# Optimization experiments

Measured on AMD Instinct MI355X. Metric: run time of the kernel, lower is better.

## Reference

```python
import math
import jax, jax.numpy as jnp
import numpy as np

B, T, C, H = 1, 2048, 1024, 16
D = C // H
ROPE_THETA = 10000.0


def rope_sin_cos(t, d, theta, dtype=jnp.float32):
    # (T, D/2) sin/cos tables, standard RoPE frequencies
    inv_freq = 1.0 / (theta ** (jnp.arange(0, d, 2, dtype=jnp.float32) / d))
    ang = jnp.arange(t, dtype=jnp.float32)[:, None] * inv_freq[None, :]  # (T, D/2)
    return jnp.sin(ang).astype(dtype), jnp.cos(ang).astype(dtype)


def apply_rope(x, sin, cos):
    # x: (B, H, T, D); rotate interleaved even/odd pairs
    x1 = x[..., 0::2]
    x2 = x[..., 1::2]
    s = sin[None, None, :, :]
    c = cos[None, None, :, :]
    r1 = x1 * c - x2 * s
    r2 = x1 * s + x2 * c
    # interleave back to (..., D)
    return jnp.stack([r1, r2], axis=-1).reshape(x.shape)


def setup_inputs() -> dict:
    key = jax.random.key(0)
    k1, k2, k3 = jax.random.split(key, 3)
    x = jax.random.normal(k1, (B, T, C), dtype=jnp.float32)
    w_qkv = jax.random.normal(k2, (C, 3 * C), dtype=jnp.float32) * (1.0 / math.sqrt(C))
    w_proj = jax.random.normal(k3, (C, C), dtype=jnp.float32) * (1.0 / math.sqrt(C))
    return {"x": x, "w_qkv": w_qkv, "w_proj": w_proj}


def reference(x, w_qkv, w_proj):
    b, t, c = x.shape
    qkv = x @ w_qkv                               # (B, T, 3C)
    qkv = qkv.reshape(b, t, 3, H, D)
    q = qkv[:, :, 0].transpose(0, 2, 1, 3)        # (B, H, T, D)
    k = qkv[:, :, 1].transpose(0, 2, 1, 3)
    v = qkv[:, :, 2].transpose(0, 2, 1, 3)

    sin, cos = rope_sin_cos(t, D, ROPE_THETA, dtype=x.dtype)
    q = apply_rope(q, sin, cos)
    k = apply_rope(k, sin, cos)

    scores = jnp.einsum('bhqd,bhkd->bhqk', q, k) * (1.0 / math.sqrt(D))
    causal = jnp.tril(jnp.ones((t, t), dtype=bool))
    scores = jnp.where(causal[None, None, :, :], scores, jnp.finfo(scores.dtype).min)
    probs = jax.nn.softmax(scores, axis=-1)       # (B, H, T, T)
    out = jnp.einsum('bhqk,bhkd->bhqd', probs, v)
    out = out.transpose(0, 2, 1, 3).reshape(b, t, c)
    return out @ w_proj
```

## Files before the change

### kernel.cpp

```cpp
#include <hip/hip_runtime.h>
#include <math.h>

#define TT 2048
#define CC 1024
#define HH 16
#define DD 64
#define N3 3072

typedef unsigned short u16;
typedef __bf16 bf16x8 __attribute__((ext_vector_type(8)));
typedef float f32x4 __attribute__((ext_vector_type(4)));
typedef unsigned short u16x8 __attribute__((ext_vector_type(8)));
typedef const __attribute__((address_space(1))) void gv_t;
typedef __attribute__((address_space(3))) void lv_t;

__device__ __forceinline__ u16 bf16_rne(float f) {
  unsigned u = __float_as_uint(f);
  u += 0x7FFFu + ((u >> 16) & 1u);
  return (u16)(u >> 16);
}
__device__ __forceinline__ float bf16f(u16 h) {
  return __uint_as_float(((unsigned)h) << 16);
}
__device__ __forceinline__ bf16x8 ldfrag(const u16* p) {
  return __builtin_bit_cast(bf16x8, *(const u16x8*)p);
}
#if __has_builtin(__builtin_amdgcn_cvt_pk_bf16_f32)
__device__ __forceinline__ unsigned pk_bf16(float a, float b) {
  return __builtin_bit_cast(unsigned, __builtin_amdgcn_cvt_pk_bf16_f32(a, b));
}
#else
__device__ __forceinline__ unsigned pk_bf16(float a, float b) {
  return (unsigned)bf16_rne(a) | ((unsigned)bf16_rne(b) << 16);
}
#endif

__global__ __launch_bounds__(256) void k_prep(
    const float* __restrict__ x, const float* __restrict__ w_qkv,
    const float* __restrict__ w_proj, u16* __restrict__ xb,
    u16* __restrict__ wqkvT, u16* __restrict__ wprojT,
    float2* __restrict__ scos ) {
  __shared__ u16 tile[64][34];
  const int bi = blockIdx.x, tid = threadIdx.x;
  if (bi < 2048) {
    int i = bi * 256 + tid;
    float4 v = ((const float4*)x)[i];
    ushort4 r;
    r.x = bf16_rne(v.x); r.y = bf16_rne(v.y); r.z = bf16_rne(v.z); r.w = bf16_rne(v.w);
    ((ushort4*)xb)[i] = r;
    return;
  }
  if (bi >= 2048 + 1536 + 512) {
    int idx = (bi - 4096) * 256 + tid;
    int t = idx >> 5, i = idx & 31;
    float inv_freq = exp2f(-(float)(2 * i) * (1.0f / 64.0f) * 13.2877123795494f);
    float ang = (float)t * inv_freq;
    scos[idx] = make_float2(sinf(ang), cosf(ang));
    return;
  }
  const float* w; u16* wt; int K, N, n0, k0;
  if (bi < 2048 + 1536) {
    int b = bi - 2048; w = w_qkv; wt = wqkvT; K = CC; N = N3;
    k0 = (b / 96) * 64; n0 = (b % 96) * 32;
  } else {
    int b = bi - 3584; w = w_proj; wt = wprojT; K = CC; N = CC;
    k0 = (b >> 5) * 64; n0 = (b & 31) * 32;
  }
  const int tx = tid & 31, r0 = tid >> 5;
#pragma unroll
  for (int j = 0; j < 8; j++) {
    int k = r0 + j * 8;
    tile[k][tx] = bf16_rne(w[(size_t)(k0 + k) * N + n0 + tx]);
  }
  __syncthreads();
  const int kc = tid & 15, nr = tid >> 4;
#pragma unroll
  for (int jn = 0; jn < 2; jn++) {
    int n = nr + (jn << 4);
    ushort4 o;
    o.x = tile[kc * 4 + 0][n];
    o.y = tile[kc * 4 + 1][n];
    o.z = tile[kc * 4 + 2][n];
    o.w = tile[kc * 4 + 3][n];
    *(ushort4*)&wt[(size_t)(n0 + n) * K + k0 + kc * 4] = o;
  }
}

__device__ __forceinline__ bf16x8 rdsw(const u16* base, int rr, int c8) {
  return ldfrag(&base[rr * 64 + ((c8 ^ (rr & 7)) << 3)]);
}

__global__ __launch_bounds__(256) void k_gemm_qkv(
    const u16* __restrict__ A, const u16* __restrict__ Bt,
    const float2* __restrict__ scos , u16* __restrict__ qr,
    u16* __restrict__ kr, u16* __restrict__ vt, int M, int N, int K) {
  __shared__ u16 As[2][128 * 64];
  __shared__ u16 Bs[2][96 * 64];
  const int tid = threadIdx.x;
  const int lane = tid & 63, w = tid >> 6;
  const int col = lane & 15, quad = lane >> 4;
  const int wm = w >> 1, wn = w & 1;
  const int tm = blockIdx.y * 128, tn = blockIdx.x * 96;

  const int lr = lane >> 3;
  const int soff = ((lane & 7) ^ lr) << 3;

  f32x4 acc[12];
#pragma unroll
  for (int i = 0; i < 12; i++) acc[i] = (f32x4){0.f, 0.f, 0.f, 0.f};

  auto stage = [&](int k0, int buf) {
#pragma unroll
    for (int i = 0; i < 4; i++) {
      const int rbase = w * 32 + i * 8;
      __builtin_amdgcn_global_load_lds(
          (gv_t*)(A + (size_t)(tm + rbase + lr) * K + k0 + soff),
          (lv_t*)(&As[buf][rbase * 64]), 16, 0, 0);
    }
#pragma unroll
    for (int i = 0; i < 3; i++) {
      const int rbase = w * 24 + i * 8;
      __builtin_amdgcn_global_load_lds(
          (gv_t*)(Bt + (size_t)(tn + rbase + lr) * K + k0 + soff),
          (lv_t*)(&Bs[buf][rbase * 64]), 16, 0, 0);
    }
  };

  stage(0, 0);
  __syncthreads();
  const int NT = K / 64;
  for (int t = 0; t < NT; t++) {
    const int cur = t & 1;
    if (t + 1 < NT) stage((t + 1) * 64, cur ^ 1);
#pragma unroll
    for (int kk = 0; kk < 2; kk++) {
      bf16x8 af[4], bf[3];
#pragma unroll
      for (int mt = 0; mt < 4; mt++)
        af[mt] = rdsw(&As[cur][0], wm * 64 + mt * 16 + col, kk * 4 + quad);
#pragma unroll
      for (int nt = 0; nt < 3; nt++)
        bf[nt] = rdsw(&Bs[cur][0], wn * 48 + nt * 16 + col, kk * 4 + quad);
#pragma unroll
      for (int mt = 0; mt < 4; mt++)
#pragma unroll
        for (int nt = 0; nt < 3; nt++)
          acc[mt * 3 + nt] = __builtin_amdgcn_mfma_f32_16x16x32_bf16(af[mt], bf[nt], acc[mt * 3 + nt], 0, 0, 0);
    }
    __syncthreads();
  }
  u16* scr = ((u16*)As) + w * 1088;

  const int tb = tm + wm * 64;
#pragma unroll
  for (int nt = 0; nt < 3; nt++) {
    const int nn = tn + wn * 48 + nt * 16;
    const int slice = nn >> 10;
    const int hh = (nn >> 6) & 15;
    const int db = nn & 63;
    const int d = db + col;
    if (slice < 2) {
      u16* dst = (slice == 0) ? qr : kr;
      const bool ev = (col & 1) == 0;
      const int i = (db >> 1) + (col >> 1);
#pragma unroll
      for (int mt = 0; mt < 4; mt++)
#pragma unroll
        for (int r = 0; r < 4; r++) {
          int t = tb + mt * 16 + quad * 4 + r;
          float2 sc2 = scos[t * 32 + i];
          float e = acc[mt * 3 + nt][r];
          float pp = __shfl_xor(e, 1);
          float v = ev ? (e * sc2.y - pp * sc2.x) : (pp * sc2.x + e * sc2.y);
          dst[((size_t)(hh * TT + t) << 6) + d] = bf16_rne(v);
        }
    } else {
#pragma unroll
      for (int mt = 0; mt < 4; mt++)
#pragma unroll
        for (int r = 0; r < 4; r++)
          scr[col * 68 + mt * 16 + quad * 4 + r] = bf16_rne(acc[mt * 3 + nt][r]);
#pragma unroll
      for (int i = 0; i < 4; i++) {
        const int dl = quad + i * 4;
        const int tl = col * 4;
        ushort4 vv = *(const ushort4*)&scr[dl * 68 + tl];
        *(ushort4*)&vt[((size_t)(hh * DD + db + dl)) * TT + tb + tl] = vv;
      }
    }
  }
}

__global__ __launch_bounds__(256) void k_gemm_pj(
    const u16* __restrict__ A, const u16* __restrict__ Bt,
    float* __restrict__ C, int M, int N, int K) {
  __shared__ u16 As[2][128 * 64];
  __shared__ u16 Bs[2][64 * 64];
  const int tid = threadIdx.x;
  const int lane = tid & 63, w = tid >> 6;
  const int col = lane & 15, quad = lane >> 4;
  const int tm = blockIdx.y * 128, tn = blockIdx.x * 64;

  const int lr = lane >> 3;
  const int soff = ((lane & 7) ^ lr) << 3;

  f32x4 acc[8];
#pragma unroll
  for (int i = 0; i < 8; i++) acc[i] = (f32x4){0.f, 0.f, 0.f, 0.f};

  auto stage = [&](int k0, int buf) {
#pragma unroll
    for (int i = 0; i < 4; i++) {
      const int rbase = w * 32 + i * 8;
      __builtin_amdgcn_global_load_lds(
          (gv_t*)(A + (size_t)(tm + rbase + lr) * K + k0 + soff),
          (lv_t*)(&As[buf][rbase * 64]), 16, 0, 0);
    }
#pragma unroll
    for (int i = 0; i < 2; i++) {
      const int rbase = w * 16 + i * 8;
      __builtin_amdgcn_global_load_lds(
          (gv_t*)(Bt + (size_t)(tn + rbase + lr) * K + k0 + soff),
          (lv_t*)(&Bs[buf][rbase * 64]), 16, 0, 0);
    }
  };

  stage(0, 0);
  __syncthreads();
  const int NT = K / 64;
  for (int t = 0; t < NT; t++) {
    const int cur = t & 1;
    if (t + 1 < NT) stage((t + 1) * 64, cur ^ 1);
#pragma unroll
    for (int kk = 0; kk < 2; kk++) {
      bf16x8 af[2], bf[4];
#pragma unroll
      for (int mt = 0; mt < 2; mt++)
        af[mt] = rdsw(&As[cur][0], w * 32 + mt * 16 + col, kk * 4 + quad);
#pragma unroll
      for (int nt = 0; nt < 4; nt++)
        bf[nt] = rdsw(&Bs[cur][0], nt * 16 + col, kk * 4 + quad);
#pragma unroll
      for (int mt = 0; mt < 2; mt++)
#pragma unroll
        for (int nt = 0; nt < 4; nt++)
          acc[mt * 4 + nt] = __builtin_amdgcn_mfma_f32_16x16x32_bf16(af[mt], bf[nt], acc[mt * 4 + nt], 0, 0, 0);
    }
    __syncthreads();
  }
#pragma unroll
  for (int mt = 0; mt < 2; mt++)
#pragma unroll
    for (int nt = 0; nt < 4; nt++)
#pragma unroll
      for (int r = 0; r < 4; r++)
        C[(size_t)(tm + w * 32 + mt * 16 + quad * 4 + r) * N + tn + nt * 16 + col] =
            acc[mt * 4 + nt][r];
}

__global__ __launch_bounds__(256) void k_flash(
    const u16* __restrict__ qr, const u16* __restrict__ kr,
    const u16* __restrict__ vt, u16* __restrict__ attnb ) {
  __shared__ u16 Ks[2][2][64 * 64];
  __shared__ u16 Vs[2][2][64 * 64];
  __shared__ u16 Ps[4][16 * 64];

  const int tid = threadIdx.x;
  const int lane = tid & 63, wv = tid >> 6;
  const int col = lane & 15, quad = lane >> 4;

  const int bid = blockIdx.x;
  const int xcd = bid & 7, slot = bid >> 3;
  const int cu = slot & 31, half = slot >> 5;
  const int rank = half ? (63 - cu) : cu;
  const int sp = 31 - (rank >> 1);
  const int h = xcd * 2 + (rank & 1);
  const int q0 = sp * 64;
  const int nkt = sp + 1;
  const int nw = (nkt + 1) >> 1;

  const u16* Qh = qr + (size_t)h * TT * DD;
  const u16* Kh = kr + (size_t)h * TT * DD;
  const u16* Vh = vt + (size_t)h * DD * TT;

  const bf16x8 aq0 = ldfrag(&Qh[(size_t)(q0 + wv * 16 + col) * DD + quad * 8]);
  const bf16x8 aq1 = ldfrag(&Qh[(size_t)(q0 + wv * 16 + col) * DD + 32 + quad * 8]);

  const int lr = lane >> 3;
  const int srcoff = ((lane & 7) ^ lr) << 3;

  auto stage = [&](int win, int buf) {
    const int k0 = win * 128;
#pragma unroll
    for (int j = 0; j < 2; j++) {
#pragma unroll
      for (int i = 0; i < 2; i++) {
        const int rbase = wv * 16 + i * 8;
        __builtin_amdgcn_global_load_lds(
            (gv_t*)(Kh + (size_t)(k0 + j * 64 + rbase + lr) * DD + srcoff),
            (lv_t*)(&Ks[buf][j][rbase * 64]), 16, 0, 0);
        __builtin_amdgcn_global_load_lds(
            (gv_t*)(Vh + (size_t)(rbase + lr) * TT + k0 + j * 64 + srcoff),
            (lv_t*)(&Vs[buf][j][rbase * 64]), 16, 0, 0);
      }
    }
  };

  const f32x4 zero = {0.f, 0.f, 0.f, 0.f};
  f32x4 acc[4] = {zero, zero, zero, zero};
  float lpart[4] = {0.f, 0.f, 0.f, 0.f};
  u16* Pb = &Ps[wv][0];

  auto compute = [&](int k0j, const u16* Kt, const u16* Vt) {
    f32x4 sc[4];
#pragma unroll
    for (int nt = 0; nt < 4; nt++) {
      const int rr = nt * 16 + col;
      sc[nt] = __builtin_amdgcn_mfma_f32_16x16x32_bf16(aq0, rdsw(Kt, rr, quad), zero, 0, 0, 0);
      sc[nt] = __builtin_amdgcn_mfma_f32_16x16x32_bf16(aq1, rdsw(Kt, rr, 4 + quad), sc[nt], 0, 0, 0);
    }
    if (k0j == q0) {
#pragma unroll
      for (int nt = 0; nt < 4; nt++)
#pragma unroll
        for (int r = 0; r < 4; r++)
          if (nt * 16 + col > wv * 16 + quad * 4 + r) sc[nt][r] = -1e30f;
    }
#pragma unroll
    for (int nt = 0; nt < 4; nt++)
#pragma unroll
      for (int r = 0; r < 4; r++) {
        float p = exp2f(fmaf(sc[nt][r], 0.18033688f, -28.8539008f));
        sc[nt][r] = p;
        lpart[r] += p;
      }
#pragma unroll
    for (int nt = 0; nt < 4; nt++) {
      unsigned p01 = pk_bf16(sc[nt][0], sc[nt][1]);
      unsigned p23 = pk_bf16(sc[nt][2], sc[nt][3]);
      u16* base = Pb + quad * 4 * 64 + ((nt ^ quad) << 4) + col;
      base[0 * 64] = (u16)p01;
      base[1 * 64] = (u16)(p01 >> 16);
      base[2 * 64] = (u16)p23;
      base[3 * 64] = (u16)(p23 >> 16);
    }
#pragma unroll
    for (int kk = 0; kk < 2; kk++) {
      int sb = (kk * 2 + (quad >> 1)) ^ (col >> 2);
      bf16x8 ap = ldfrag(&Pb[col * 64 + (sb << 4) + ((quad & 1) << 3)]);
#pragma unroll
      for (int nt = 0; nt < 4; nt++)
        acc[nt] = __builtin_amdgcn_mfma_f32_16x16x32_bf16(
            ap, rdsw(Vt, nt * 16 + col, kk * 4 + quad), acc[nt], 0, 0, 0);
    }
  };

  stage(0, 0);
  for (int win = 0; win < nw; win++) {
    const int buf = win & 1;
    __syncthreads();
    if (win + 1 < nw) stage(win + 1, buf ^ 1);
#pragma unroll
    for (int j = 0; j < 2; j++) {
      const int k0j = win * 128 + j * 64;
      if (k0j <= q0) compute(k0j, Ks[buf][j], Vs[buf][j]);
    }
  }

#pragma unroll
  for (int o = 1; o < 16; o <<= 1)
#pragma unroll
    for (int r = 0; r < 4; r++) lpart[r] += __shfl_xor(lpart[r], o);
  float inv[4];
#pragma unroll
  for (int r = 0; r < 4; r++) inv[r] = 1.f / lpart[r];
#pragma unroll
  for (int nt = 0; nt < 4; nt++)
#pragma unroll
    for (int r = 0; r < 4; r++) {
      int q = q0 + wv * 16 + quad * 4 + r;
      attnb[(size_t)q * CC + h * DD + nt * 16 + col] = bf16_rne(acc[nt][r] * inv[r]);
    }
}

extern "C" void kernel_launch(void* const* d_in, const int* in_sizes, int n_in,
                              void* d_out, int out_size, void* d_ws, size_t ws_size,
                              hipStream_t stream) {
  const float* x      = (const float*)d_in[0];
  const float* w_qkv  = (const float*)d_in[1];
  const float* w_proj = (const float*)d_in[2];
  float* out = (float*)d_out;

  char* p = (char*)d_ws;
  u16* xb      = (u16*)p;    p += (size_t)TT * CC * 2;
  u16* wqkvT   = (u16*)p;    p += (size_t)N3 * CC * 2;
  u16* wprojT  = (u16*)p;    p += (size_t)CC * CC * 2;
  float2* scos = (float2*)p; p += (size_t)TT * 32 * 8;
  u16* qr      = (u16*)p;    p += (size_t)HH * TT * DD * 2;
  u16* kr      = (u16*)p;    p += (size_t)HH * TT * DD * 2;
  u16* vt      = (u16*)p;    p += (size_t)HH * DD * TT * 2;
  u16* attnb   = (u16*)p;    p += (size_t)TT * CC * 2;

  k_prep<<<2048 + 1536 + 512 + 256, 256, 0, stream>>>(x, w_qkv, w_proj, xb, wqkvT, wprojT, scos);
  k_gemm_qkv<<<dim3(N3 / 96, TT / 128), 256, 0, stream>>>(xb, wqkvT, scos, qr, kr, vt, TT, N3, CC);
  k_flash<<<512, 256, 0, stream>>>(qr, kr, vt, attnb);
  k_gemm_pj<<<dim3(CC / 64, TT / 128), 256, 0, stream>>>(attnb, wprojT, out, TT, CC, CC);
}
```

Baseline: 143.9 us.

## Load K/V fragments directly from global memory in flash kernel, dropping LDS staging

Removes the double-buffered LDS staging of K and V tiles (global_load_lds plus __syncthreads) and has each wave read its MFMA B-operand fragments straight from global memory. This removes block-wide barriers and 64KB of shared memory, which could raise occupancy. In exchange, each of the four waves fetches the same K/V data independently, so it relies on L1/L2 hits and loses the software prefetch overlap, exposing global load latency inside the inner loop.

```diff
diff --git a/kernel.cpp b/kernel.cpp
--- a/kernel.cpp
+++ b/kernel.cpp
@@ -261,8 +261,6 @@
 __global__ __launch_bounds__(256) void k_flash(
     const u16* __restrict__ qr, const u16* __restrict__ kr,
     const u16* __restrict__ vt, u16* __restrict__ attnb ) {
-  __shared__ u16 Ks[2][2][64 * 64];
-  __shared__ u16 Vs[2][2][64 * 64];
   __shared__ u16 Ps[4][16 * 64];
 
   const int tid = threadIdx.x;
@@ -276,8 +274,6 @@
   const int sp = 31 - (rank >> 1);
   const int h = xcd * 2 + (rank & 1);
   const int q0 = sp * 64;
-  const int nkt = sp + 1;
-  const int nw = (nkt + 1) >> 1;
 
   const u16* Qh = qr + (size_t)h * TT * DD;
   const u16* Kh = kr + (size_t)h * TT * DD;
@@ -285,39 +281,20 @@
 
   const bf16x8 aq0 = ldfrag(&Qh[(size_t)(q0 + wv * 16 + col) * DD + quad * 8]);
   const bf16x8 aq1 = ldfrag(&Qh[(size_t)(q0 + wv * 16 + col) * DD + 32 + quad * 8]);
-
-  const int lr = lane >> 3;
-  const int srcoff = ((lane & 7) ^ lr) << 3;
-
-  auto stage = [&](int win, int buf) {
-    const int k0 = win * 128;
-#pragma unroll
-    for (int j = 0; j < 2; j++) {
-#pragma unroll
-      for (int i = 0; i < 2; i++) {
-        const int rbase = wv * 16 + i * 8;
-        __builtin_amdgcn_global_load_lds(
-            (gv_t*)(Kh + (size_t)(k0 + j * 64 + rbase + lr) * DD + srcoff),
-            (lv_t*)(&Ks[buf][j][rbase * 64]), 16, 0, 0);
-        __builtin_amdgcn_global_load_lds(
-            (gv_t*)(Vh + (size_t)(rbase + lr) * TT + k0 + j * 64 + srcoff),
-            (lv_t*)(&Vs[buf][j][rbase * 64]), 16, 0, 0);
-      }
-    }
-  };
 
   const f32x4 zero = {0.f, 0.f, 0.f, 0.f};
   f32x4 acc[4] = {zero, zero, zero, zero};
   float lpart[4] = {0.f, 0.f, 0.f, 0.f};
   u16* Pb = &Ps[wv][0];
 
-  auto compute = [&](int k0j, const u16* Kt, const u16* Vt) {
+  for (int k0j = 0; k0j <= q0; k0j += 64) {
     f32x4 sc[4];
 #pragma unroll
     for (int nt = 0; nt < 4; nt++) {
       const int rr = nt * 16 + col;
-      sc[nt] = __builtin_amdgcn_mfma_f32_16x16x32_bf16(aq0, rdsw(Kt, rr, quad), zero, 0, 0, 0);
-      sc[nt] = __builtin_amdgcn_mfma_f32_16x16x32_bf16(aq1, rdsw(Kt, rr, 4 + quad), sc[nt], 0, 0, 0);
+      const u16* krow = &Kh[(size_t)(k0j + rr) * DD];
+      sc[nt] = __builtin_amdgcn_mfma_f32_16x16x32_bf16(aq0, ldfrag(&krow[quad * 8]), zero, 0, 0, 0);
+      sc[nt] = __builtin_amdgcn_mfma_f32_16x16x32_bf16(aq1, ldfrag(&krow[32 + quad * 8]), sc[nt], 0, 0, 0);
     }
     if (k0j == q0) {
 #pragma unroll
@@ -349,21 +326,10 @@
       int sb = (kk * 2 + (quad >> 1)) ^ (col >> 2);
       bf16x8 ap = ldfrag(&Pb[col * 64 + (sb << 4) + ((quad & 1) << 3)]);
 #pragma unroll
-      for (int nt = 0; nt < 4; nt++)
-        acc[nt] = __builtin_amdgcn_mfma_f32_16x16x32_bf16(
-            ap, rdsw(Vt, nt * 16 + col, kk * 4 + quad), acc[nt], 0, 0, 0);
-    }
-  };
-
-  stage(0, 0);
-  for (int win = 0; win < nw; win++) {
-    const int buf = win & 1;
-    __syncthreads();
-    if (win + 1 < nw) stage(win + 1, buf ^ 1);
-#pragma unroll
-    for (int j = 0; j < 2; j++) {
-      const int k0j = win * 128 + j * 64;
-      if (k0j <= q0) compute(k0j, Ks[buf][j], Vs[buf][j]);
+      for (int nt = 0; nt < 4; nt++) {
+        bf16x8 bv = ldfrag(&Vh[(size_t)(nt * 16 + col) * TT + k0j + kk * 32 + quad * 8]);
+        acc[nt] = __builtin_amdgcn_mfma_f32_16x16x32_bf16(ap, bv, acc[nt], 0, 0, 0);
+      }
     }
   }
 
```

After: 178.5 us. 1.24x slower.
